# Kernel tuning notes

Measured on AMD Instinct MI355X. Metric: run time of the kernel, lower is better.

## Reference

```python
import jax, jax.numpy as jnp
import numpy as np

B, S, D, H = 2, 2048, 1024, 16
DH = D // H  # head_dim = 64


def setup_inputs() -> dict:
    key = jax.random.key(0)
    ks = jax.random.split(key, 12)
    sd = 0.02
    return {
        "query": jax.random.normal(ks[0], (B, S, D), jnp.float32),
        "value": jax.random.normal(ks[1], (B, S, D), jnp.float32),
        "Wq": jax.random.normal(ks[2], (D, D), jnp.float32) * sd,
        "bq": jnp.zeros((D,), jnp.float32),
        "Wk": jax.random.normal(ks[3], (D, DH), jnp.float32) * sd,
        "bk": jnp.zeros((DH,), jnp.float32),
        "Wv": jax.random.normal(ks[4], (D, DH), jnp.float32) * sd,
        "bv": jnp.zeros((DH,), jnp.float32),
        "Wo": jax.random.normal(ks[5], (D, D), jnp.float32) * sd,
        "bo": jnp.zeros((D,), jnp.float32),
    }


def reference(query, value, Wq, bq, Wk, bk, Wv, bv, Wo, bo):
    b, s, d = query.shape
    # per-head queries: (B, H, S, DH)
    Q = (query @ Wq + bq).reshape(b, s, H, DH).transpose(0, 2, 1, 3)
    # single shared K/V head: (B, S, DH)
    K = value @ Wk + bk
    V = value @ Wv + bv
    scale = 1.0 / jnp.sqrt(jnp.asarray(DH, Q.dtype))
    # broadcast shared K over all query heads: (B, H, S, S)
    scores = jnp.einsum("bhsd,btd->bhst", Q, K) * scale
    weights = jax.nn.softmax(scores, axis=-1)
    # (B, H, S, DH)
    attn = jnp.einsum("bhst,btd->bhsd", weights, V)
    concat = attn.transpose(0, 2, 1, 3).reshape(b, s, d)
    return concat @ Wo + bo
```

## Files before the change

kernel.cpp:

```cpp
#include <hip/hip_runtime.h>
#include <hip/hip_bf16.h>
#include <cstdint>

#define S_LEN 2048
#define D_MODEL 1024
#define NHEAD 16
#define DHEAD 64
#define BATCH 2

typedef __attribute__((ext_vector_type(4))) __bf16 bf16x4v;
typedef __attribute__((ext_vector_type(8))) __bf16 bf16x8v;
typedef __attribute__((ext_vector_type(16))) float f32x16;
typedef const __attribute__((address_space(1))) uint32_t gu32;
typedef __attribute__((address_space(3))) uint32_t lu32;

#define QSCALE 0.18033688011112042f

__device__ __forceinline__ int perm4(int gidx) {
    return (gidx & ~3) | ((gidx & 1) << 1) | ((gidx >> 1) & 1);
}
__device__ __forceinline__ int permk(int k) {
    return (k & ~12) | ((k & 4) << 1) | ((k & 8) >> 1);
}

__global__ __launch_bounds__(256) void prep_all(
    const float* __restrict__ query,
    const float* __restrict__ Wq, const float* __restrict__ Wo,
    const float* __restrict__ Wk, const float* __restrict__ Wv,
    __hip_bfloat16* __restrict__ Qin,
    __hip_bfloat16* __restrict__ Wqt, __hip_bfloat16* __restrict__ Wohit,
    __hip_bfloat16* __restrict__ Wkvt)
{
    const int bid = blockIdx.x;
    const int tid = threadIdx.x;
    if (bid < 4096) {
        const int idx = bid * 256 + tid;
        const float4 v = reinterpret_cast<const float4*>(query)[idx];
        bf16x4v o = { (__bf16)v.x, (__bf16)v.y, (__bf16)v.z, (__bf16)v.w };
        *reinterpret_cast<bf16x4v*>(Qin + (size_t)perm4(idx) * 4) = o;
        return;
    }
    const int b2 = bid - 4096;
    const int bx = b2 & 31, by = (b2 >> 5) & 31, z = b2 >> 10;
    const float* W;
    __hip_bfloat16* T;
    int wcols, trowoff;
    if (z == 0)      { W = Wq; T = Wqt;   wcols = 1024; trowoff = 0; }
    else if (z == 1) { W = Wo; T = Wohit; wcols = 1024; trowoff = 0; }
    else if (z == 2) { W = Wk; T = Wkvt;  wcols = 64;   trowoff = 0; }
    else             { W = Wv; T = Wkvt;  wcols = 64;   trowoff = 64; }
    if (bx * 32 >= wcols) return;

    __shared__ float ld[32][33];
    {
        const int rr = tid >> 3;
        const int c4 = (tid & 7) * 4;
        const float4 v = *reinterpret_cast<const float4*>(
            &W[(size_t)(by * 32 + rr) * wcols + bx * 32 + c4]);
        ld[rr][c4 + 0] = v.x; ld[rr][c4 + 1] = v.y;
        ld[rr][c4 + 2] = v.z; ld[rr][c4 + 3] = v.w;
    }
    __syncthreads();
    const int jj = tid & 31;
#pragma unroll
    for (int ii = 0; ii < 4; ++ii) {
        const int rr = (tid >> 5) * 4 + ii;
        T[(size_t)(trowoff + bx * 32 + rr) * 1024 + by * 32 + permk(jj)] =
            __float2bfloat16(ld[jj][rr]);
    }
}

__global__ __launch_bounds__(512, 1) void qproj_projkv(
    const __hip_bfloat16* __restrict__ Qin,
    const __hip_bfloat16* __restrict__ Wqt,
    const float* __restrict__ bq,
    __hip_bfloat16* __restrict__ Qbf,
    const float* __restrict__ value,
    const __hip_bfloat16* __restrict__ Wkvt,
    const float* __restrict__ bk, const float* __restrict__ bv,
    __hip_bfloat16* __restrict__ Kb,
    __hip_bfloat16* __restrict__ Vt)
{
    __shared__ __align__(16) char lds[131072];
    const int bid = blockIdx.x;
    const int tid = threadIdx.x;

    if (bid < 64) {
        const int unit = tid >> 8;
        const int ltid = tid & 255;
        const int w = ltid >> 6, lane = ltid & 63;
        const int g = lane >> 5, r = lane & 31;
        const int rowBase = bid * 64 + unit * 32;
        char* ub = lds + unit * 65536;

        auto stage = [&](int buf, int t) {
            const int kk = t * 64;
            char* dst = ub + buf * 24576;
#pragma unroll
            for (int j = 0; j < 2; ++j) {
                const int oo  = j * 4096 + ltid * 16;
                const int row = oo >> 8;
                const int cb  = (oo & 255) ^ ((row & 7) << 4);
                __builtin_amdgcn_global_load_lds(
                    (gu32*)((const char*)value + (size_t)(rowBase + row) * 4096 + kk * 4 + cb),
                    (lu32*)(dst + oo), 16, 0, 0);
            }
#pragma unroll
            for (int j = 0; j < 4; ++j) {
                const int oo  = j * 4096 + ltid * 16;
                const int row = oo >> 7;
                const int cb  = (oo & 127) ^ ((row & 7) << 4);
                __builtin_amdgcn_global_load_lds(
                    (gu32*)((const char*)Wkvt + (size_t)row * 2048 + kk * 2 + cb),
                    (lu32*)(dst + 8192 + oo), 16, 0, 0);
            }
        };

        f32x16 acc;
#pragma unroll
        for (int i = 0; i < 16; ++i) acc[i] = 0.f;

        stage(0, 0);

        for (int t = 0; t < 16; ++t) {
            const int cur = t & 1;
            if (t < 15) {
                stage(cur ^ 1, t + 1);
                asm volatile("s_waitcnt vmcnt(6)" ::: "memory");
            } else {
                asm volatile("s_waitcnt vmcnt(0)" ::: "memory");
            }
            asm volatile("s_barrier" ::: "memory");

            const char* ab = ub + cur * 24576;
            const char* bb = ab + 8192;

#pragma unroll
            for (int ks = 0; ks < 4; ++ks) {
                const int sza = (r & 7) << 4;
                const char* pa = ab + r * 256;
                const float4 x0 = *reinterpret_cast<const float4*>(
                    pa + ((ks * 64 + g * 16) ^ sza));
                const float4 x1 = *reinterpret_cast<const float4*>(
                    pa + ((ks * 64 + 32 + g * 16) ^ sza));
                bf16x8v af = {(__bf16)x0.x, (__bf16)x0.y, (__bf16)x0.z, (__bf16)x0.w,
                              (__bf16)x1.x, (__bf16)x1.y, (__bf16)x1.z, (__bf16)x1.w};
                bf16x8v bf = *reinterpret_cast<const bf16x8v*>(
                    bb + (w * 32 + r) * 128 + ((ks * 32 + g * 16) ^ sza));
                acc = __builtin_amdgcn_mfma_f32_32x32x16_bf16(af, bf, acc, 0, 0, 0);
            }
            asm volatile("s_barrier" ::: "memory");
        }

        __syncthreads();
        float* ep = reinterpret_cast<float*>(ub);
#pragma unroll
        for (int reg = 0; reg < 16; ++reg) {
            const int m = (reg & 3) + 8 * (reg >> 2) + 4 * g;
            ep[m * 132 + w * 32 + r] = acc[reg];
        }
        __syncthreads();

        {
            const int m  = ltid >> 3;
            const int g0 = (ltid & 7) * 2;
#pragma unroll
            for (int j = 0; j < 2; ++j) {
                const int gsrc = g0 + j;
                bf16x4v o4;
#pragma unroll
                for (int i2 = 0; i2 < 4; ++i2)
                    o4[i2] = (__bf16)(ep[m * 132 + gsrc * 4 + i2] + bk[gsrc * 4 + i2]);
                *reinterpret_cast<bf16x4v*>(
                    Kb + (size_t)(rowBase + m) * 64 + perm4(gsrc) * 4) = o4;
            }
        }
        {
            const int vc = ltid >> 2;
            const int g0 = (ltid & 3) * 2;
            const int batch = rowBase >> 11;
            const float bvv = bv[vc];
#pragma unroll
            for (int j = 0; j < 2; ++j) {
                const int gsrc = g0 + j;
                bf16x4v o4;
#pragma unroll
                for (int i2 = 0; i2 < 4; ++i2)
                    o4[i2] = (__bf16)(ep[(gsrc * 4 + i2) * 132 + 64 + vc] + bvv);
                *reinterpret_cast<bf16x4v*>(
                    Vt + ((size_t)(batch * 64 + vc)) * 2048 + (rowBase & 2047) + perm4(gsrc) * 4) = o4;
            }
        }
        return;
    }

    const int lin = bid - 64;
    const int w = tid >> 6, lane = tid & 63;
    const int g = lane >> 5, r = lane & 31;
    const int wr = w >> 2, wc = w & 3;
    const int swz = (lin & 7) * 32 + (lin >> 3);
    const int rowBase = (swz >> 3) * 128;
    const int colBase = (swz & 7) * 128;

    auto stage = [&](int buf, int t) {
        const int kk = t * 64;
        char* dst = lds + buf * 32768;
#pragma unroll
        for (int j = 0; j < 2; ++j) {
            const int oo  = j * 8192 + tid * 16;
            const int row = oo >> 7;
            const int cb  = (oo & 127) ^ ((row & 7) << 4);
            __builtin_amdgcn_global_load_lds(
                (gu32*)((const char*)Qin + (size_t)(rowBase + row) * 2048 + kk * 2 + cb),
                (lu32*)(dst + oo), 16, 0, 0);
            __builtin_amdgcn_global_load_lds(
                (gu32*)((const char*)Wqt + (size_t)(colBase + row) * 2048 + kk * 2 + cb),
                (lu32*)(dst + 16384 + oo), 16, 0, 0);
        }
    };

    f32x16 acc[2];
#pragma unroll
    for (int i = 0; i < 16; ++i) { acc[0][i] = 0.f; acc[1][i] = 0.f; }

    stage(0, 0); stage(1, 1); stage(2, 2);

    for (int t = 0; t < 16; ++t) {
        if (t <= 13)      { asm volatile("s_waitcnt vmcnt(8)" ::: "memory"); }
        else if (t == 14) { asm volatile("s_waitcnt vmcnt(4)" ::: "memory"); }
        else              { asm volatile("s_waitcnt vmcnt(0)" ::: "memory"); }
        asm volatile("s_barrier" ::: "memory");

        if (t + 3 < 16) stage((t + 3) & 3, t + 3);

        const char* ahb = lds + (t & 3) * 32768;
        const char* bb  = ahb + 16384;

        __builtin_amdgcn_s_setprio(1);
#pragma unroll
        for (int ks = 0; ks < 4; ++ks) {
            bf16x8v a[2], bfr;
#pragma unroll
            for (int mt = 0; mt < 2; ++mt) {
                const int rowl = wr * 64 + mt * 32 + r;
                const int sz = (rowl & 7) << 4;
                a[mt] = *reinterpret_cast<const bf16x8v*>(
                    ahb + rowl * 128 + ((ks * 32 + g * 16) ^ sz));
            }
            {
                const int rowl = wc * 32 + r;
                const int sz = (rowl & 7) << 4;
                bfr = *reinterpret_cast<const bf16x8v*>(
                    bb + rowl * 128 + ((ks * 32 + g * 16) ^ sz));
            }
#pragma unroll
            for (int mt = 0; mt < 2; ++mt)
                acc[mt] = __builtin_amdgcn_mfma_f32_32x32x16_bf16(a[mt], bfr, acc[mt], 0, 0, 0);
        }
        __builtin_amdgcn_s_setprio(0);
    }

    const int col = colBase + wc * 32 + r;
    const int colp = permk(col);
    const float bvv = bq[col];
#pragma unroll
    for (int mt = 0; mt < 2; ++mt)
#pragma unroll
        for (int reg = 0; reg < 16; ++reg) {
            const int row = rowBase + wr * 64 + mt * 32 + (reg & 3) + 8 * (reg >> 2) + 4 * g;
            Qbf[(size_t)row * 1024 + colp] =
                (__hip_bfloat16)((acc[mt][reg] + bvv) * QSCALE);
        }
}

__global__ __launch_bounds__(512, 1) void gemm_oproj(
    const __hip_bfloat16* __restrict__ A,
    const __hip_bfloat16* __restrict__ Bhi,
    const float* __restrict__ bias, float* __restrict__ C)
{
    __shared__ __align__(16) char lds[131072];

    const int tid = threadIdx.x;
    const int w = tid >> 6, lane = tid & 63;
    const int g = lane >> 5, r = lane & 31;
    const int wr = w >> 2, wc = w & 3;
    const int lin = blockIdx.y * 8 + blockIdx.x;
    const int swz = (lin & 7) * 32 + (lin >> 3);
    const int rowBase = (swz >> 3) * 128;
    const int colBase = (swz & 7) * 128;

    auto stage = [&](int buf, int t) {
        const int kk = t * 64;
        char* dst = lds + buf * 32768;
#pragma unroll
        for (int j = 0; j < 2; ++j) {
            const int oo  = j * 8192 + tid * 16;
            const int row = oo >> 7;
            const int cb  = (oo & 127) ^ ((row & 7) << 4);
            __builtin_amdgcn_global_load_lds(
                (gu32*)((const char*)A + (size_t)(rowBase + row) * 2048 + kk * 2 + cb),
                (lu32*)(dst + oo), 16, 0, 0);
            __builtin_amdgcn_global_load_lds(
                (gu32*)((const char*)Bhi + (size_t)(colBase + row) * 2048 + kk * 2 + cb),
                (lu32*)(dst + 16384 + oo), 16, 0, 0);
        }
    };

    f32x16 acc[2];
#pragma unroll
    for (int i = 0; i < 16; ++i) { acc[0][i] = 0.f; acc[1][i] = 0.f; }

    stage(0, 0); stage(1, 1); stage(2, 2);

    for (int t = 0; t < 16; ++t) {
        if (t <= 13)      { asm volatile("s_waitcnt vmcnt(8)" ::: "memory"); }
        else if (t == 14) { asm volatile("s_waitcnt vmcnt(4)" ::: "memory"); }
        else              { asm volatile("s_waitcnt vmcnt(0)" ::: "memory"); }
        asm volatile("s_barrier" ::: "memory");

        if (t + 3 < 16) stage((t + 3) & 3, t + 3);

        const char* ahb = lds + (t & 3) * 32768;
        const char* bb  = ahb + 16384;

        __builtin_amdgcn_s_setprio(1);
#pragma unroll
        for (int ks = 0; ks < 4; ++ks) {
            bf16x8v a[2], bfr;
#pragma unroll
            for (int mt = 0; mt < 2; ++mt) {
                const int rowl = wr * 64 + mt * 32 + r;
                const int sz = (rowl & 7) << 4;
                a[mt] = *reinterpret_cast<const bf16x8v*>(
                    ahb + rowl * 128 + ((ks * 32 + g * 16) ^ sz));
            }
            {
                const int rowl = wc * 32 + r;
                const int sz = (rowl & 7) << 4;
                bfr = *reinterpret_cast<const bf16x8v*>(
                    bb + rowl * 128 + ((ks * 32 + g * 16) ^ sz));
            }
#pragma unroll
            for (int mt = 0; mt < 2; ++mt)
                acc[mt] = __builtin_amdgcn_mfma_f32_32x32x16_bf16(a[mt], bfr, acc[mt], 0, 0, 0);
        }
        __builtin_amdgcn_s_setprio(0);
    }

    const int col = colBase + wc * 32 + r;
    const float bvv = bias[col];
#pragma unroll
    for (int mt = 0; mt < 2; ++mt)
#pragma unroll
        for (int reg = 0; reg < 16; ++reg) {
            const int row = rowBase + wr * 64 + mt * 32 + (reg & 3) + 8 * (reg >> 2) + 4 * g;
            C[(size_t)row * 1024 + col] = acc[mt][reg] + bvv;
        }
}

__global__ __launch_bounds__(256, 2) void mqa_attn_mfma(
    const __hip_bfloat16* __restrict__ Qbf,
    const __hip_bfloat16* __restrict__ Kbf,
    const __hip_bfloat16* __restrict__ Vt,
    __hip_bfloat16* __restrict__ Ahi)
{
    __shared__ __align__(16) char lds[65536];

    const int bh = blockIdx.y, b = bh >> 4, h = bh & 15;
    const int qt = blockIdx.x;
    const int tid = threadIdx.x;
    const int w = tid >> 6, lane = tid & 63;
    const int g = lane >> 5, q = lane & 31;

    bf16x8v qf[4];
    {
        const __hip_bfloat16* qp =
            Qbf + ((size_t)(b * S_LEN + qt * 128 + w * 32 + q)) * D_MODEL + h * DHEAD;
#pragma unroll
        for (int ks = 0; ks < 4; ++ks)
            qf[ks] = *reinterpret_cast<const bf16x8v*>(qp + ks * 16 + g * 8);
    }

    const bf16x8v onesf = {(__bf16)1.f, (__bf16)1.f, (__bf16)1.f, (__bf16)1.f,
                           (__bf16)1.f, (__bf16)1.f, (__bf16)1.f, (__bf16)1.f};
    f32x16 fzero;
#pragma unroll
    for (int i = 0; i < 16; ++i) fzero[i] = 0.f;

    int koff[2][4], voff[2][4];
#pragma unroll
    for (int mt = 0; mt < 2; ++mt) {
        const int key = mt * 32 + q;
        const int swzk = (key & 7) << 4;
#pragma unroll
        for (int ks = 0; ks < 4; ++ks) {
            koff[mt][ks] = key * 128 + ((ks * 32 + g * 16) ^ swzk);
            voff[mt][ks] = 8192 + key * 128 + ((ks * 32 + g * 16) ^ swzk);
        }
    }

    const char* kbase = (const char*)Kbf + (size_t)b * S_LEN * DHEAD * 2;
    const char* vbase = (const char*)Vt + (size_t)b * DHEAD * S_LEN * 2;

    auto stage = [&](int buf, int t0) {
        char* dst = lds + buf * 16384;
#pragma unroll
        for (int j = 0; j < 2; ++j) {
            const int oo = j * 4096 + tid * 16;
            const int rr = oo >> 7;
            const int cc = (oo & 127) ^ ((rr & 7) << 4);
            __builtin_amdgcn_global_load_lds(
                (gu32*)(kbase + (size_t)(t0 + rr) * 128 + cc),
                (lu32*)(dst + oo), 16, 0, 0);
            __builtin_amdgcn_global_load_lds(
                (gu32*)(vbase + (size_t)rr * (S_LEN * 2) + t0 * 2 + cc),
                (lu32*)(dst + 8192 + oo), 16, 0, 0);
        }
    };

    f32x16 oacc[2], oacc_l;
#pragma unroll
    for (int i = 0; i < 16; ++i) { oacc[0][i] = 0.f; oacc[1][i] = 0.f; oacc_l[i] = 0.f; }

    auto qkt = [&](f32x16 (&SD)[2], int buf) {
        const char* kb_ = lds + buf * 16384;
#pragma unroll
        for (int mt = 0; mt < 2; ++mt) {
            bf16x8v af0 = *reinterpret_cast<const bf16x8v*>(kb_ + koff[mt][0]);
            SD[mt] = __builtin_amdgcn_mfma_f32_32x32x16_bf16(af0, qf[0], fzero, 0, 0, 0);
#pragma unroll
            for (int ks = 1; ks < 4; ++ks) {
                bf16x8v af = *reinterpret_cast<const bf16x8v*>(kb_ + koff[mt][ks]);
                SD[mt] = __builtin_amdgcn_mfma_f32_32x32x16_bf16(af, qf[ks], SD[mt], 0, 0, 0);
            }
        }
    };

    auto smpv = [&](f32x16 (&SD)[2], int buf) {
#pragma unroll
        for (int mt = 0; mt < 2; ++mt)
#pragma unroll
            for (int r2 = 0; r2 < 16; ++r2)
                SD[mt][r2] = exp2f(SD[mt][r2]);

        bf16x8v pf[4];
#pragma unroll
        for (int ks = 0; ks < 4; ++ks)
#pragma unroll
            for (int e2 = 0; e2 < 8; ++e2)
                pf[ks][e2] = (__bf16)SD[ks >> 1][(ks & 1) * 8 + e2];

        const char* kb_ = lds + buf * 16384;
#pragma unroll
        for (int mt = 0; mt < 2; ++mt) {
#pragma unroll
            for (int ks = 0; ks < 4; ++ks) {
                bf16x8v af = *reinterpret_cast<const bf16x8v*>(kb_ + voff[mt][ks]);
                oacc[mt] = __builtin_amdgcn_mfma_f32_32x32x16_bf16(af, pf[ks], oacc[mt], 0, 0, 0);
            }
        }
#pragma unroll
        for (int ks = 0; ks < 4; ++ks)
            oacc_l = __builtin_amdgcn_mfma_f32_32x32x16_bf16(onesf, pf[ks], oacc_l, 0, 0, 0);
    };

    f32x16 sA[2], sB[2];

    stage(0, 0); stage(1, 64); stage(2, 128);
    asm volatile("s_waitcnt vmcnt(8)" ::: "memory");
    asm volatile("s_barrier" ::: "memory");
    qkt(sA, 0);

#define BODY(SB_, TILE_, BQ_, BP_, CUR, NXT, VMCSTR, DOSTAGE)               \
    {                                                                        \
        asm volatile("s_waitcnt vmcnt(" VMCSTR ")" ::: "memory");            \
        asm volatile("s_barrier" ::: "memory");                              \
        if (DOSTAGE) stage(SB_, TILE_);                                      \
        qkt(NXT, BQ_);                                                       \
        smpv(CUR, BP_);                                                      \
    }

    for (int ib = 0; ib < 7; ++ib) {
        const int t4 = ib * 4;
        BODY(3, (t4 + 3) * 64, 1, 0, sA, sB, "4", true);
        BODY(0, (t4 + 4) * 64, 2, 1, sB, sA, "4", true);
        BODY(1, (t4 + 5) * 64, 3, 2, sA, sB, "4", true);
        BODY(2, (t4 + 6) * 64, 0, 3, sB, sA, "4", true);
    }
    BODY(3, 31 * 64, 1, 0, sA, sB, "4", true);
    BODY(0, 0,       2, 1, sB, sA, "4", false);
    BODY(0, 0,       3, 2, sA, sB, "0", false);
#undef BODY
    smpv(sB, 3);

    const float inv = 1.f / oacc_l[0];
    __syncthreads();
    {
        float* ep = reinterpret_cast<float*>(lds) + w * 2080;
#pragma unroll
        for (int mt = 0; mt < 2; ++mt)
#pragma unroll
            for (int r = 0; r < 16; ++r) {
                const int d = mt * 32 + (r & 3) + ((r >> 2) * 8) + g * 4;
                ep[q * 65 + d] = oacc[mt][r] * inv;
            }
    }
    __syncthreads();

    const size_t obase = (size_t)(b * S_LEN + qt * 128) * D_MODEL + h * DHEAD;
    for (int i = tid; i < 128 * 16; i += 256) {
        const int rloc = i >> 4, G = i & 15;
        const float* src = reinterpret_cast<float*>(lds) + (rloc >> 5) * 2080 + (rloc & 31) * 65 + G * 4;
        const size_t o = obase + (size_t)rloc * D_MODEL + perm4(G) * 4;
        bf16x4v hv;
#pragma unroll
        for (int j = 0; j < 4; ++j) hv[j] = (__bf16)src[j];
        *reinterpret_cast<bf16x4v*>(Ahi + o) = hv;
    }
}

extern "C" void kernel_launch(void* const* d_in, const int* in_sizes, int n_in,
                              void* d_out, int out_size, void* d_ws, size_t ws_size,
                              hipStream_t stream)
{
    const float* query = (const float*)d_in[0];
    const float* value = (const float*)d_in[1];
    const float* Wq    = (const float*)d_in[2];
    const float* bq    = (const float*)d_in[3];
    const float* Wk    = (const float*)d_in[4];
    const float* bk    = (const float*)d_in[5];
    const float* Wv    = (const float*)d_in[6];
    const float* bv    = (const float*)d_in[7];
    const float* Wo    = (const float*)d_in[8];
    const float* bo    = (const float*)d_in[9];
    float* out = (float*)d_out;

    char* ws = (char*)d_ws;
    const size_t MB = 1024 * 1024;
    __hip_bfloat16* Qin   = (__hip_bfloat16*)(ws);
    __hip_bfloat16* Qbf   = (__hip_bfloat16*)(ws + 8 * MB);
    __hip_bfloat16* Abuf  = (__hip_bfloat16*)(ws + 8 * MB);
    __hip_bfloat16* Wqt   = (__hip_bfloat16*)(ws + 16 * MB);
    __hip_bfloat16* Kbf   = (__hip_bfloat16*)(ws + 18 * MB);
    __hip_bfloat16* Vt    = (__hip_bfloat16*)(ws + 18 * MB + 524288);
    __hip_bfloat16* Wohit = (__hip_bfloat16*)(ws + 19 * MB);
    __hip_bfloat16* Wkvt  = (__hip_bfloat16*)(ws + 21 * MB);

    prep_all<<<dim3(8192), dim3(256), 0, stream>>>(
        query, Wq, Wo, Wk, Wv, Qin, Wqt, Wohit, Wkvt);

    qproj_projkv<<<dim3(320), dim3(512), 0, stream>>>(
        Qin, Wqt, bq, Qbf, value, Wkvt, bk, bv, Kbf, Vt);

    mqa_attn_mfma<<<dim3(S_LEN / 128, BATCH * NHEAD), dim3(256), 0, stream>>>(
        Qbf, Kbf, Vt, Abuf);

    gemm_oproj<<<dim3(8, 32), dim3(512), 0, stream>>>(
        Abuf, Wohit, bo, out);
}
```

Before: 100.6 us.

## Process two query sub-tiles per wave in MQA attention to reuse K/V fragments

Each attention block now covers 256 query rows instead of 128, with every wave holding two 32-row query sub-tiles. Each K/V fragment read from LDS feeds two MFMAs, which halves LDS reads and global K/V staging per query row. The cost is roughly double the accumulator and score registers, so launch bounds drop to one block per SIMD pair. The grid shrinks to 256 blocks, which may leave some of the GPU's compute units idle.

```diff
diff --git a/kernel.cpp b/kernel.cpp
--- a/kernel.cpp
+++ b/kernel.cpp
@@ -358,7 +358,7 @@
         }
 }
 
-__global__ __launch_bounds__(256, 2) void mqa_attn_mfma(
+__global__ __launch_bounds__(256, 1) void mqa_attn_mfma(
     const __hip_bfloat16* __restrict__ Qbf,
     const __hip_bfloat16* __restrict__ Kbf,
     const __hip_bfloat16* __restrict__ Vt,
@@ -372,13 +372,14 @@
     const int w = tid >> 6, lane = tid & 63;
     const int g = lane >> 5, q = lane & 31;
 
-    bf16x8v qf[4];
-    {
+    bf16x8v qf[2][4];
+#pragma unroll
+    for (int su = 0; su < 2; ++su) {
         const __hip_bfloat16* qp =
-            Qbf + ((size_t)(b * S_LEN + qt * 128 + w * 32 + q)) * D_MODEL + h * DHEAD;
+            Qbf + ((size_t)(b * S_LEN + qt * 256 + w * 64 + su * 32 + q)) * D_MODEL + h * DHEAD;
 #pragma unroll
         for (int ks = 0; ks < 4; ++ks)
-            qf[ks] = *reinterpret_cast<const bf16x8v*>(qp + ks * 16 + g * 8);
+            qf[su][ks] = *reinterpret_cast<const bf16x8v*>(qp + ks * 16 + g * 8);
     }
 
     const bf16x8v onesf = {(__bf16)1.f, (__bf16)1.f, (__bf16)1.f, (__bf16)1.f,
@@ -418,37 +419,47 @@
         }
     };
 
-    f32x16 oacc[2], oacc_l;
-#pragma unroll
-    for (int i = 0; i < 16; ++i) { oacc[0][i] = 0.f; oacc[1][i] = 0.f; oacc_l[i] = 0.f; }
-
-    auto qkt = [&](f32x16 (&SD)[2], int buf) {
+    f32x16 oacc[2][2], oacc_l[2];
+#pragma unroll
+    for (int i = 0; i < 16; ++i) {
+        oacc[0][0][i] = 0.f; oacc[0][1][i] = 0.f;
+        oacc[1][0][i] = 0.f; oacc[1][1][i] = 0.f;
+        oacc_l[0][i] = 0.f;  oacc_l[1][i] = 0.f;
+    }
+
+    auto qkt = [&](f32x16 (&SD)[2][2], int buf) {
         const char* kb_ = lds + buf * 16384;
 #pragma unroll
         for (int mt = 0; mt < 2; ++mt) {
             bf16x8v af0 = *reinterpret_cast<const bf16x8v*>(kb_ + koff[mt][0]);
-            SD[mt] = __builtin_amdgcn_mfma_f32_32x32x16_bf16(af0, qf[0], fzero, 0, 0, 0);
+            SD[0][mt] = __builtin_amdgcn_mfma_f32_32x32x16_bf16(af0, qf[0][0], fzero, 0, 0, 0);
+            SD[1][mt] = __builtin_amdgcn_mfma_f32_32x32x16_bf16(af0, qf[1][0], fzero, 0, 0, 0);
 #pragma unroll
             for (int ks = 1; ks < 4; ++ks) {
                 bf16x8v af = *reinterpret_cast<const bf16x8v*>(kb_ + koff[mt][ks]);
-                SD[mt] = __builtin_amdgcn_mfma_f32_32x32x16_bf16(af, qf[ks], SD[mt], 0, 0, 0);
+                SD[0][mt] = __builtin_amdgcn_mfma_f32_32x32x16_bf16(af, qf[0][ks], SD[0][mt], 0, 0, 0);
+                SD[1][mt] = __builtin_amdgcn_mfma_f32_32x32x16_bf16(af, qf[1][ks], SD[1][mt], 0, 0, 0);
             }
         }
     };
 
-    auto smpv = [&](f32x16 (&SD)[2], int buf) {
-#pragma unroll
-        for (int mt = 0; mt < 2; ++mt)
-#pragma unroll
-            for (int r2 = 0; r2 < 16; ++r2)
-                SD[mt][r2] = exp2f(SD[mt][r2]);
-
-        bf16x8v pf[4];
-#pragma unroll
-        for (int ks = 0; ks < 4; ++ks)
-#pragma unroll
-            for (int e2 = 0; e2 < 8; ++e2)
-                pf[ks][e2] = (__bf16)SD[ks >> 1][(ks & 1) * 8 + e2];
+    auto smpv = [&](f32x16 (&SD)[2][2], int buf) {
+#pragma unroll
+        for (int su = 0; su < 2; ++su)
+#pragma unroll
+            for (int mt = 0; mt < 2; ++mt)
+#pragma unroll
+                for (int r2 = 0; r2 < 16; ++r2)
+                    SD[su][mt][r2] = exp2f(SD[su][mt][r2]);
+
+        bf16x8v pf[2][4];
+#pragma unroll
+        for (int su = 0; su < 2; ++su)
+#pragma unroll
+            for (int ks = 0; ks < 4; ++ks)
+#pragma unroll
+                for (int e2 = 0; e2 < 8; ++e2)
+                    pf[su][ks][e2] = (__bf16)SD[su][ks >> 1][(ks & 1) * 8 + e2];
 
         const char* kb_ = lds + buf * 16384;
 #pragma unroll
@@ -456,15 +467,18 @@
 #pragma unroll
             for (int ks = 0; ks < 4; ++ks) {
                 bf16x8v af = *reinterpret_cast<const bf16x8v*>(kb_ + voff[mt][ks]);
-                oacc[mt] = __builtin_amdgcn_mfma_f32_32x32x16_bf16(af, pf[ks], oacc[mt], 0, 0, 0);
-            }
-        }
-#pragma unroll
-        for (int ks = 0; ks < 4; ++ks)
-            oacc_l = __builtin_amdgcn_mfma_f32_32x32x16_bf16(onesf, pf[ks], oacc_l, 0, 0, 0);
+                oacc[0][mt] = __builtin_amdgcn_mfma_f32_32x32x16_bf16(af, pf[0][ks], oacc[0][mt], 0, 0, 0);
+                oacc[1][mt] = __builtin_amdgcn_mfma_f32_32x32x16_bf16(af, pf[1][ks], oacc[1][mt], 0, 0, 0);
+            }
+        }
+#pragma unroll
+        for (int su = 0; su < 2; ++su)
+#pragma unroll
+            for (int ks = 0; ks < 4; ++ks)
+                oacc_l[su] = __builtin_amdgcn_mfma_f32_32x32x16_bf16(onesf, pf[su][ks], oacc_l[su], 0, 0, 0);
     };
 
-    f32x16 sA[2], sB[2];
+    f32x16 sA[2][2], sB[2][2];
 
     stage(0, 0); stage(1, 64); stage(2, 128);
     asm volatile("s_waitcnt vmcnt(8)" ::: "memory");
@@ -493,29 +507,34 @@
 #undef BODY
     smpv(sB, 3);
 
-    const float inv = 1.f / oacc_l[0];
-    __syncthreads();
-    {
-        float* ep = reinterpret_cast<float*>(lds) + w * 2080;
-#pragma unroll
-        for (int mt = 0; mt < 2; ++mt)
-#pragma unroll
-            for (int r = 0; r < 16; ++r) {
-                const int d = mt * 32 + (r & 3) + ((r >> 2) * 8) + g * 4;
-                ep[q * 65 + d] = oacc[mt][r] * inv;
-            }
-    }
-    __syncthreads();
-
-    const size_t obase = (size_t)(b * S_LEN + qt * 128) * D_MODEL + h * DHEAD;
-    for (int i = tid; i < 128 * 16; i += 256) {
-        const int rloc = i >> 4, G = i & 15;
-        const float* src = reinterpret_cast<float*>(lds) + (rloc >> 5) * 2080 + (rloc & 31) * 65 + G * 4;
-        const size_t o = obase + (size_t)rloc * D_MODEL + perm4(G) * 4;
-        bf16x4v hv;
-#pragma unroll
-        for (int j = 0; j < 4; ++j) hv[j] = (__bf16)src[j];
-        *reinterpret_cast<bf16x4v*>(Ahi + o) = hv;
+    const float inv[2] = { 1.f / oacc_l[0][0], 1.f / oacc_l[1][0] };
+    const size_t obase = (size_t)(b * S_LEN + qt * 256) * D_MODEL + h * DHEAD;
+
+#pragma unroll
+    for (int su = 0; su < 2; ++su) {
+        __syncthreads();
+        {
+            float* ep = reinterpret_cast<float*>(lds) + w * 2080;
+#pragma unroll
+            for (int mt = 0; mt < 2; ++mt)
+#pragma unroll
+                for (int r = 0; r < 16; ++r) {
+                    const int d = mt * 32 + (r & 3) + ((r >> 2) * 8) + g * 4;
+                    ep[q * 65 + d] = oacc[su][mt][r] * inv[su];
+                }
+        }
+        __syncthreads();
+
+        for (int i = tid; i < 128 * 16; i += 256) {
+            const int rloc = i >> 4, G = i & 15;
+            const int wv = rloc >> 5, rw = rloc & 31;
+            const float* src = reinterpret_cast<float*>(lds) + wv * 2080 + rw * 65 + G * 4;
+            const size_t o = obase + (size_t)(wv * 64 + su * 32 + rw) * D_MODEL + perm4(G) * 4;
+            bf16x4v hv;
+#pragma unroll
+            for (int j = 0; j < 4; ++j) hv[j] = (__bf16)src[j];
+            *reinterpret_cast<bf16x4v*>(Ahi + o) = hv;
+        }
     }
 }
 
@@ -552,7 +571,7 @@
     qproj_projkv<<<dim3(320), dim3(512), 0, stream>>>(
         Qin, Wqt, bq, Qbf, value, Wkvt, bk, bv, Kbf, Vt);
 
-    mqa_attn_mfma<<<dim3(S_LEN / 128, BATCH * NHEAD), dim3(256), 0, stream>>>(
+    mqa_attn_mfma<<<dim3(S_LEN / 256, BATCH * NHEAD), dim3(256), 0, stream>>>(
         Qbf, Kbf, Vt, Abuf);
 
     gemm_oproj<<<dim3(8, 32), dim3(512), 0, stream>>>(
```

After: 109.1 us. 1.09x slower.
